# Kernel optimization log

Hardware: AMD Instinct MI355X
Metric: run time of the kernel (lower is better)

## Reference

```python
import jax, jax.numpy as jnp
import numpy as np

# Social pooling hyperparameters (from init_kwargs config)
INFLUENCE_RADIUS = 10.0
SIGMA = 5.0
MAX_NEIGHBORS = 32
COORD_SCALE = 100.0  # coordinates uniform in [0, 100)^2


def setup_inputs() -> dict:
    key = jax.random.key(0)
    k1, k2 = jax.random.split(key)
    B, N, D = 8, 8192, 64
    features = jax.random.normal(k1, (B, N, D), dtype=jnp.float32)
    coordinates = jax.random.uniform(k2, (N, 2), dtype=jnp.float32) * COORD_SCALE
    return {"features": features, "coordinates": coordinates}


def _spatial_weights(coordinates):
    # Pairwise squared Euclidean distances [N, N]
    diff = coordinates[:, None, :] - coordinates[None, :, :]
    d2 = jnp.sum(diff * diff, axis=-1)
    d = jnp.sqrt(jnp.maximum(d2, 1e-12))
    # Gaussian kernel with hard radius cutoff
    w = jnp.exp(-d2 / (2.0 * SIGMA * SIGMA))
    w = jnp.where(d <= INFLUENCE_RADIUS, w, 0.0)
    # Neighbor limit: keep top-k weights per row
    topk_vals, _ = jax.lax.top_k(w, MAX_NEIGHBORS)  # [N, K]
    thresh = topk_vals[:, -1:]
    w = jnp.where(w >= thresh, w, 0.0)
    # weighted_mean normalization
    row_sums = jnp.clip(jnp.sum(w, axis=1, keepdims=True), 1e-8, None)
    return w / row_sums


def reference(features, coordinates):
    # features: [B, N, D]; coordinates: [N, 2]
    weights = _spatial_weights(coordinates)          # [N, N]
    pooled = jnp.einsum('ij,bjd->bid', weights, features)
    return pooled  # aggregation_layer is Identity (learnable_aggregation=False)
```

## Files before the change

### kernel.cpp

```cpp
#include <hip/hip_runtime.h>
#include <math.h>


constexpr int   NCELL  = 10;
constexpr int   NCELL2 = 100;
constexpr int   MAXC   = 416;
constexpr int   MAXK   = 64;
constexpr float BUCKSC = 2.56f;
constexpr int   NXCD   = 8;

__device__ __forceinline__ int cell_x(float x) {
    int c = (int)(x * 0.09765625f);
    return min(max(c, 0), NCELL - 1);
}
__device__ __forceinline__ int cell_of(float2 c) {
    return cell_x(c.y) * NCELL + cell_x(c.x);
}

__device__ __forceinline__ void wsync() {
    __builtin_amdgcn_wave_barrier();
    __threadfence_block();
    __builtin_amdgcn_wave_barrier();
}

__global__ __launch_bounds__(1024)
void k_prep(const float* __restrict__ C, int* __restrict__ cellStart,
            float2* __restrict__ bXY, int* __restrict__ bIdx, int N)
{
    __shared__ int h[128];
    __shared__ int cur[NCELL2];
    const int t = threadIdx.x;
    if (t < 128) h[t] = 0;
    __syncthreads();
    const float2* C2 = (const float2*)C;
    for (int j = t; j < N; j += 1024) atomicAdd(&h[cell_of(C2[j])], 1);
    __syncthreads();
    #pragma unroll
    for (int o = 1; o < 128; o <<= 1) {
        int u = (t < 128 && t >= o) ? h[t - o] : 0;
        __syncthreads();
        if (t < 128) h[t] += u;
        __syncthreads();
    }
    if (t < NCELL2) {
        int s = (t == 0) ? 0 : h[t - 1];
        cur[t] = s; cellStart[t] = s;
        if (t == 0) cellStart[NCELL2] = h[NCELL2 - 1];
    }
    __syncthreads();
    for (int j = t; j < N; j += 1024) {
        float2 c = C2[j];
        int pos = atomicAdd(&cur[cell_of(c)], 1);
        bXY[pos] = c; bIdx[pos] = j;
    }
}

template<int TN, int TB>
__global__ __launch_bounds__(256, 8)
void social_pool_main(const float* __restrict__ F,
                      const float2* __restrict__ bXY,
                      const int* __restrict__ bIdx,
                      const int* __restrict__ cellStart,
                      float* __restrict__ out, int Nrt, int Brt)
{
    const int N = (TN > 0) ? TN : Nrt;
    const int B = (TB > 0) ? TB : Brt;

    __shared__ float  s_cd2[4][MAXC];
    __shared__ int    s_cjj[4][MAXC];
    __shared__ __align__(16) int s_hist[4][256];
    __shared__ float  s_blist[4][32];
    __shared__ float2 s_kwj[4][MAXK];

    const int t = threadIdx.x, wid = t >> 6, lane = t & 63;
    float*  cd2   = s_cd2[wid];
    int*    cjj   = s_cjj[wid];
    int*    hist  = s_hist[wid];
    float*  blist = s_blist[wid];
    float2* kwj   = s_kwj[wid];

    *(int4*)&hist[lane * 4] = make_int4(0, 0, 0, 0);

    const int bid = blockIdx.x, nb = gridDim.x;
    const int sb = (nb % NXCD == 0) ? (bid % NXCD) * (nb / NXCD) + bid / NXCD : bid;
    const int q = sb * 4 + wid;
    if (q >= N) return;

    const float2 ci = bXY[q];
    const int    i  = bIdx[q];
    const int cx = cell_x(ci.x), cy = cell_x(ci.y);
    const unsigned long long below = (1ull << lane) - 1ull;

    int mc = 0;
    for (int ry = max(cy - 1, 0); ry <= min(cy + 1, NCELL - 1); ++ry) {
        const int c0 = ry * NCELL + max(cx - 1, 0);
        const int c1 = ry * NCELL + min(cx + 1, NCELL - 1);
        const int s = cellStart[c0], e = cellStart[c1 + 1];
        for (int p0 = s; p0 < e; p0 += 64) {
            const int p = p0 + lane;
            bool hit = false; float d2 = 0.0f; int jj = 0;
            if (p < e) {
                float2 cp = bXY[p];
                float dx = ci.x - cp.x, dy = ci.y - cp.y;
                d2 = dx * dx + dy * dy;
                float d = sqrtf(fmaxf(d2, 1e-12f));
                if (d <= 10.0f) { hit = true; jj = bIdx[p]; }
            }
            unsigned long long mk = __ballot(hit);
            int off = __popcll(mk & below);
            if (hit && mc + off < MAXC) { cd2[mc + off] = d2; cjj[mc + off] = jj; }
            mc += (int)__popcll(mk);
        }
    }
    wsync();
    const int M = min(mc, MAXC);

    float thr_d2, thr_w;
    if (M > 32) {
        for (int k = lane; k < M; k += 64)
            atomicAdd(&hist[min(255, (int)(cd2[k] * BUCKSC))], 1);
        wsync();
        int4 h4 = *(const int4*)&hist[lane * 4];
        int hh0 = h4.x, hh1 = h4.y, hh2 = h4.z, hh3 = h4.w;
        int tot = hh0 + hh1 + hh2 + hh3;
        int sc = tot;
        #pragma unroll
        for (int o = 1; o < 64; o <<= 1) {
            int v = __shfl_up(sc, o);
            if (lane >= o) sc += v;
        }
        int ce = sc - tot;
        int fb = -1, fce = 0;
        if (ce <= 31 && 31 < ce + hh0) { fb = lane * 4 + 0; fce = ce; } ce += hh0;
        if (fb < 0 && ce <= 31 && 31 < ce + hh1) { fb = lane * 4 + 1; fce = ce; } ce += hh1;
        if (fb < 0 && ce <= 31 && 31 < ce + hh2) { fb = lane * 4 + 2; fce = ce; } ce += hh2;
        if (fb < 0 && ce <= 31 && 31 < ce + hh3) { fb = lane * 4 + 3; fce = ce; }
        unsigned long long mk1 = __ballot(fb >= 0);
        int src1 = (mk1 != 0ull) ? (__ffsll((unsigned long long)mk1) - 1) : 0;
        const int bstar   = __shfl(fb,  src1);
        const int cumexcl = __shfl(fce, src1);
        int bn = 0;
        for (int k0 = 0; k0 < M; k0 += 64) {
            const int k = k0 + lane;
            bool inb = (k < M) && (min(255, (int)(cd2[k] * BUCKSC)) == bstar);
            unsigned long long mk = __ballot(inb);
            int off = __popcll(mk & below);
            if (inb && bn + off < 32) blist[bn + off] = cd2[k];
            bn += (int)__popcll(mk);
        }
        wsync();
        bn = min(bn, 32);
        float mine = 0.0f; int ok = 0;
        if (lane < bn) {
            mine = blist[lane];
            int cl = 0, ceq = 0;
            for (int m = 0; m < bn; ++m) {
                cl  += (blist[m] <  mine);
                ceq += (blist[m] == mine);
            }
            int r = cumexcl + cl;
            ok = (r <= 31 && 31 < r + ceq);
        }
        unsigned long long mk2 = __ballot(ok);
        int src2 = (mk2 != 0ull) ? (__ffsll((unsigned long long)mk2) - 1) : 0;
        thr_d2 = __shfl(mine, src2);
        thr_w  = expf(-(thr_d2 / 50.0f));
    } else {
        thr_d2 = 3.4e38f;
        thr_w  = 0.0f;
    }

    const float marg = thr_d2 + 1e-4f;
    int kc = 0;
    for (int k0 = 0; k0 < M; k0 += 64) {
        const int k = k0 + lane;
        bool keep = false; float w = 0.0f; int jj = 0;
        if (k < M && cd2[k] <= marg) {
            w = expf(-(cd2[k] / 50.0f));
            if (w >= thr_w) { keep = true; jj = cjj[k]; }
        }
        unsigned long long mk = __ballot(keep);
        int off = __popcll(mk & below);
        if (keep && kc + off < MAXK)
            kwj[kc + off] = make_float2(w, __int_as_float(jj));
        kc += (int)__popcll(mk);
    }
    wsync();
    const int K = min(kc, MAXK);

    float v = (lane < K) ? kwj[lane].x : 0.0f;
    #pragma unroll
    for (int o = 32; o > 0; o >>= 1) v += __shfl_xor(v, o);
    const float ssum = fmaxf(v, 1e-8f);
    if (lane < K) kwj[lane].x = kwj[lane].x / ssum;
    wsync();

    const size_t NL = (size_t)N * 64;
    if (TB == 8) {
        const int dq = (lane & 15) * 4;
        const int bp = (lane >> 4) * 2;
        const float* Fb0 = F + (size_t)bp * NL + dq;
        const float* Fb1 = Fb0 + NL;
        float4 a0 = make_float4(0.f, 0.f, 0.f, 0.f);
        float4 a1 = make_float4(0.f, 0.f, 0.f, 0.f);
        #pragma unroll 2
        for (int k = 0; k < K; ++k) {
            float2 wj = kwj[k];
            const float w = wj.x;
            const size_t o = (size_t)__float_as_int(wj.y) * 64;
            float4 f0 = *(const float4*)(Fb0 + o);
            float4 f1 = *(const float4*)(Fb1 + o);
            a0.x += w * f0.x; a0.y += w * f0.y; a0.z += w * f0.z; a0.w += w * f0.w;
            a1.x += w * f1.x; a1.y += w * f1.y; a1.z += w * f1.z; a1.w += w * f1.w;
        }
        float* O0 = out + (size_t)bp * NL + (size_t)i * 64 + dq;
        *(float4*)O0 = a0;
        *(float4*)(O0 + NL) = a1;
    } else {
        const float* F0 = F + lane;
        float* O0 = out + (size_t)i * 64 + lane;
        for (int b = 0; b < B; ++b) {
            float a = 0.0f;
            const float* Fb = F0 + (size_t)b * NL;
            for (int k = 0; k < K; ++k) {
                float2 wj = kwj[k];
                a += wj.x * Fb[(size_t)__float_as_int(wj.y) * 64];
            }
            O0[(size_t)b * NL] = a;
        }
    }
}

extern "C" void kernel_launch(void* const* d_in, const int* in_sizes, int n_in,
                              void* d_out, int out_size, void* d_ws, size_t ws_size,
                              hipStream_t stream)
{
    const float* F = (const float*)d_in[0];
    const float* C = (const float*)d_in[1];
    float* out = (float*)d_out;

    const int N = in_sizes[1] / 2;
    const int B = in_sizes[0] / (N * 64);

    char* ws = (char*)d_ws;
    int*    cellStart = (int*)(ws + 0);
    float2* bXY       = (float2*)(ws + 512);
    int*    bIdx      = (int*)(ws + 512 + (size_t)N * 8);

    k_prep<<<1, 1024, 0, stream>>>(C, cellStart, bXY, bIdx, N);
    if (N == 8192 && B == 8)
        social_pool_main<8192, 8><<<2048, 256, 0, stream>>>(F, bXY, bIdx, cellStart, out, N, B);
    else
        social_pool_main<0, 0><<<(N + 3) / 4, 256, 0, stream>>>(F, bXY, bIdx, cellStart, out, N, B);
}
```

Baseline: 51.38 us.

## Broadcast weights via readlane, defer index gather, remap queries across XCDs

The per-wave fence is replaced by a plain LDS waitcnt. Each candidate now stores its sorted position instead of gathering bIdx for every hit, and the gather happens only for neighbors kept after the threshold. Normalized weights and indices stay in registers and are broadcast with readlane in the accumulation loop, which drops the LDS write-back, a sync and the per-iteration LDS reads. When the template size is fixed, a new block-to-query mapping spreads spatially sorted queries across XCDs. That mapping assumes N=8192 and 4 waves per block (hardcoded 1024/256 strides). Readlane with a loop-variant index may also force a scalarization cost.

New measurement: 50.71 us. No clear change (-1.3%).

```diff
diff --git a/kernel.cpp b/kernel.cpp
--- a/kernel.cpp
+++ b/kernel.cpp
@@ -19,7 +19,7 @@
 
 __device__ __forceinline__ void wsync() {
     __builtin_amdgcn_wave_barrier();
-    __threadfence_block();
+    asm volatile("s_waitcnt lgkmcnt(0)" ::: "memory");
     __builtin_amdgcn_wave_barrier();
 }
 
@@ -82,8 +82,13 @@
     *(int4*)&hist[lane * 4] = make_int4(0, 0, 0, 0);
 
     const int bid = blockIdx.x, nb = gridDim.x;
-    const int sb = (nb % NXCD == 0) ? (bid % NXCD) * (nb / NXCD) + bid / NXCD : bid;
-    const int q = sb * 4 + wid;
+    int q;
+    if (TN > 0) {
+        q = (bid & 7) * 1024 + wid * 256 + (bid >> 3);
+    } else {
+        const int sb = (nb % NXCD == 0) ? (bid % NXCD) * (nb / NXCD) + bid / NXCD : bid;
+        q = sb * 4 + wid;
+    }
     if (q >= N) return;
 
     const float2 ci = bXY[q];
@@ -98,17 +103,17 @@
         const int s = cellStart[c0], e = cellStart[c1 + 1];
         for (int p0 = s; p0 < e; p0 += 64) {
             const int p = p0 + lane;
-            bool hit = false; float d2 = 0.0f; int jj = 0;
+            bool hit = false; float d2 = 0.0f;
             if (p < e) {
                 float2 cp = bXY[p];
                 float dx = ci.x - cp.x, dy = ci.y - cp.y;
                 d2 = dx * dx + dy * dy;
                 float d = sqrtf(fmaxf(d2, 1e-12f));
-                if (d <= 10.0f) { hit = true; jj = bIdx[p]; }
+                hit = (d <= 10.0f);
             }
             unsigned long long mk = __ballot(hit);
             int off = __popcll(mk & below);
-            if (hit && mc + off < MAXC) { cd2[mc + off] = d2; cjj[mc + off] = jj; }
+            if (hit && mc + off < MAXC) { cd2[mc + off] = d2; cjj[mc + off] = p; }
             mc += (int)__popcll(mk);
         }
     }
@@ -177,7 +182,7 @@
         bool keep = false; float w = 0.0f; int jj = 0;
         if (k < M && cd2[k] <= marg) {
             w = expf(-(cd2[k] / 50.0f));
-            if (w >= thr_w) { keep = true; jj = cjj[k]; }
+            if (w >= thr_w) { keep = true; jj = bIdx[cjj[k]]; }
         }
         unsigned long long mk = __ballot(keep);
         int off = __popcll(mk & below);
@@ -188,12 +193,15 @@
     wsync();
     const int K = min(kc, MAXK);
 
-    float v = (lane < K) ? kwj[lane].x : 0.0f;
+    float2 pr = make_float2(0.0f, 0.0f);
+    if (lane < K) pr = kwj[lane];
+    float v = pr.x;
     #pragma unroll
     for (int o = 32; o > 0; o >>= 1) v += __shfl_xor(v, o);
     const float ssum = fmaxf(v, 1e-8f);
-    if (lane < K) kwj[lane].x = kwj[lane].x / ssum;
-    wsync();
+    const float wn = pr.x / ssum;
+    const int   jn = __float_as_int(pr.y);
+    const int   wi = __float_as_int(wn);
 
     const size_t NL = (size_t)N * 64;
     if (TB == 8) {
@@ -205,9 +213,8 @@
         float4 a1 = make_float4(0.f, 0.f, 0.f, 0.f);
         #pragma unroll 2
         for (int k = 0; k < K; ++k) {
-            float2 wj = kwj[k];
-            const float w = wj.x;
-            const size_t o = (size_t)__float_as_int(wj.y) * 64;
+            const float w = __int_as_float(__builtin_amdgcn_readlane(wi, k));
+            const size_t o = (size_t)__builtin_amdgcn_readlane(jn, k) * 64;
             float4 f0 = *(const float4*)(Fb0 + o);
             float4 f1 = *(const float4*)(Fb1 + o);
             a0.x += w * f0.x; a0.y += w * f0.y; a0.z += w * f0.z; a0.w += w * f0.w;
@@ -223,8 +230,9 @@
             float a = 0.0f;
             const float* Fb = F0 + (size_t)b * NL;
             for (int k = 0; k < K; ++k) {
-                float2 wj = kwj[k];
-                a += wj.x * Fb[(size_t)__float_as_int(wj.y) * 64];
+                const float w = __int_as_float(__builtin_amdgcn_readlane(wi, k));
+                const size_t o = (size_t)__builtin_amdgcn_readlane(jn, k) * 64;
+                a += w * Fb[o];
             }
             O0[(size_t)b * NL] = a;
         }
```
